# Optimization experiments

Measured on AMD Instinct MI355X. Metric: run time of the kernel, lower is better.

## Reference

```python
import jax, jax.numpy as jnp
import numpy as np

B, L, V, E_ENC, D_DEC, E_EMB = 256, 128, 4096, 1024, 1024, 512


def _lin(key, out_f, in_f, scale=0.02):
    k1, k2 = jax.random.split(key)
    return (jax.random.normal(k1, (out_f, in_f), jnp.float32) * scale,
            jax.random.normal(k2, (out_f,), jnp.float32) * scale)


def setup_inputs() -> dict:
    key = jax.random.key(0)
    ks = jax.random.split(key, 12)
    x = jax.random.normal(ks[0], (B, 1, V), jnp.float32)
    hidden = jax.random.normal(ks[1], (1, B, D_DEC), jnp.float32)
    enc_output = jax.random.normal(ks[2], (B, L, E_ENC), jnp.float32)
    W1_w, W1_b = _lin(ks[3], D_DEC, E_ENC)
    W2_w, W2_b = _lin(ks[4], D_DEC, D_DEC)
    V_w, V_b = _lin(ks[5], 1, D_DEC)
    out2emb_w, out2emb_b = _lin(ks[6], E_EMB, V)
    gru_wi, gru_bi = _lin(ks[7], 3 * D_DEC, E_EMB + E_ENC)
    gru_wh, gru_bh = _lin(ks[8], 3 * D_DEC, D_DEC)
    fc1_w, fc1_b = _lin(ks[9], E_EMB, D_DEC)
    fc2_w, fc2_b = _lin(ks[10], V, E_EMB)
    return dict(x=x, hidden=hidden, enc_output=enc_output,
                W1_w=W1_w, W1_b=W1_b, W2_w=W2_w, W2_b=W2_b, V_w=V_w, V_b=V_b,
                out2emb_w=out2emb_w, out2emb_b=out2emb_b,
                gru_wi=gru_wi, gru_wh=gru_wh, gru_bi=gru_bi, gru_bh=gru_bh,
                fc1_w=fc1_w, fc1_b=fc1_b, fc2_w=fc2_w, fc2_b=fc2_b)


def reference(x, hidden, enc_output, W1_w, W1_b, W2_w, W2_b, V_w, V_b,
              out2emb_w, out2emb_b, gru_wi, gru_wh, gru_bi, gru_bh,
              fc1_w, fc1_b, fc2_w, fc2_b):
    # --- Bahdanau additive attention ---
    h_t = hidden[-1][:, None, :]                                   # (B,1,dec)
    score = jnp.tanh(enc_output @ W1_w.T + W1_b + h_t @ W2_w.T + W2_b)  # (B,L,dec)
    attn = jax.nn.softmax(score @ V_w.T + V_b, axis=1)             # (B,L,1)
    context = jnp.sum(attn * enc_output, axis=1)                   # (B,enc)
    # --- embed previous output distribution ---
    x_emb = x @ out2emb_w.T + out2emb_b                            # (B,1,emb)
    rnn_in = jnp.concatenate([context[:, None, :], x_emb], -1)[:, 0, :]  # (B,emb+enc)
    # --- single GRU step (PyTorch gate layout r,z,n) ---
    h0 = hidden[0]
    gi = rnn_in @ gru_wi.T + gru_bi
    gh = h0 @ gru_wh.T + gru_bh
    ir, iz, inn = jnp.split(gi, 3, axis=-1)
    hr, hz, hn = jnp.split(gh, 3, axis=-1)
    r = jax.nn.sigmoid(ir + hr)
    z = jax.nn.sigmoid(iz + hz)
    n = jnp.tanh(inn + r * hn)
    h_new = (1.0 - z) * n + z * h0                                 # (B,dec)
    # --- output MLP ---
    out = jnp.tanh(h_new @ fc1_w.T + fc1_b) @ fc2_w.T + fc2_b      # (B,vocab)
    return out, h_new[None], attn
```

## Files before the change

### kernel.cpp

```cpp
#include <hip/hip_runtime.h>
#include <math.h>


#define B_   256
#define L_   128
#define V_   4096
#define ENC_ 1024
#define DEC_ 1024
#define EMB_ 512
#define MB_  1048576ull

typedef __bf16 bf16;
typedef __bf16 bf16x8 __attribute__((ext_vector_type(8)));
typedef __bf16 bf16x4 __attribute__((ext_vector_type(4)));
typedef float  f32x4  __attribute__((ext_vector_type(4)));

__device__ __forceinline__ float fast_tanh(float x) {
  float e = __builtin_amdgcn_exp2f(x * 2.88539008177792681472f);
  return 1.0f - 2.0f * __builtin_amdgcn_rcpf(e + 1.0f);
}
__device__ __forceinline__ float fast_sigmoid(float x) {
  return __builtin_amdgcn_rcpf(1.0f + __builtin_amdgcn_exp2f(-1.44269504088896f * x));
}

__device__ __forceinline__ void cp16(const void* g, void* l) {
  __builtin_amdgcn_global_load_lds(
      (const __attribute__((address_space(1))) void*)g,
      (__attribute__((address_space(3))) void*)l,
      16, 0, 0);
}

__device__ __forceinline__ bf16x8 ld8f(const float* f) {
  f32x4 a = *(const f32x4*)f;
  f32x4 b = *(const f32x4*)(f + 4);
  bf16x8 r;
  r[0] = (bf16)a[0]; r[1] = (bf16)a[1]; r[2] = (bf16)a[2]; r[3] = (bf16)a[3];
  r[4] = (bf16)b[0]; r[5] = (bf16)b[1]; r[6] = (bf16)b[2]; r[7] = (bf16)b[3];
  return r;
}


__device__ __forceinline__ void gemm64_f32(
    const float* __restrict__ A, const float* __restrict__ Brow,
    int strideA, int strideB, int kbeg, int kend, int row0,
    bf16* As, bf16* Bs, f32x4 acc[4])
{
  const int t   = threadIdx.x;
  const int lane = t & 63, w = t >> 6, q = lane >> 4, c16 = lane & 15;
  const int sr  = t >> 3, lb = t & 7;

  for (int k0 = kbeg; k0 < kend; k0 += 64) {
    bf16x8 va[2], vb[2];
#pragma unroll
    for (int ch = 0; ch < 2; ch++) {
      int r    = ch * 32 + sr;
      int gcol = k0 + ((lb ^ (r & 7)) << 3);
      va[ch] = ld8f(A    + (size_t)(row0 + r) * strideA + gcol);
      vb[ch] = ld8f(Brow + (size_t)r * strideB + gcol);
    }
#pragma unroll
    for (int ch = 0; ch < 2; ch++) {
      *(bf16x8*)&As[ch * 2048 + t * 8] = va[ch];
      *(bf16x8*)&Bs[ch * 2048 + t * 8] = vb[ch];
    }
    __syncthreads();
#pragma unroll
    for (int kkb = 0; kkb < 8; kkb += 4) {
      int rb = w * 16 + c16;
      bf16x8 bfr = *(const bf16x8*)&Bs[rb * 64 + (((kkb + q) ^ (rb & 7)) << 3)];
#pragma unroll
      for (int i = 0; i < 4; i++) {
        int ra = i * 16 + c16;
        bf16x8 af = *(const bf16x8*)&As[ra * 64 + (((kkb + q) ^ (ra & 7)) << 3)];
        acc[i] = __builtin_amdgcn_mfma_f32_16x16x32_bf16(af, bfr, acc[i], 0, 0, 0);
      }
    }
    __syncthreads();
  }
}

__global__ __launch_bounds__(256) void setup_k(
    const float* __restrict__ hidden, const float* __restrict__ W2,
    const float* __restrict__ wh, const float* __restrict__ W1_b,
    const float* __restrict__ W2_b, const float* __restrict__ gbh,
    const float* __restrict__ x, const float* __restrict__ o2e,
    const float* __restrict__ enc, const float* __restrict__ W1,
    const float* __restrict__ wi, const float* __restrict__ fc1w,
    const float* __restrict__ fc2w,
    bf16* __restrict__ enc_bf, bf16* __restrict__ W1_bf,
    bf16* __restrict__ wi_bf, bf16* __restrict__ fc1_bf,
    bf16* __restrict__ fc2_bf,
    bf16* __restrict__ u, bf16* __restrict__ gh, float* __restrict__ xe4)
{
  __shared__ __align__(16) bf16 As[64 * 64];
  __shared__ __align__(16) bf16 Bs[64 * 64];

  const int bid = blockIdx.x;
  const int t   = threadIdx.x;

  if (bid >= 384) {
    int i = bid - 384;
    const float* src; bf16* dst; int blk;
    if      (i < 8192) { src = enc;  dst = enc_bf; blk = i; }
    else if (i < 8448) { src = W1;   dst = W1_bf;  blk = i - 8192; }
    else if (i < 9600) { src = wi;   dst = wi_bf;  blk = i - 8448; }
    else if (i < 9728) { src = fc1w; dst = fc1_bf; blk = i - 9600; }
    else               { src = fc2w; dst = fc2_bf; blk = i - 9728; }
    const size_t base = (size_t)blk * 4096 + t * 16;
    const float* s = src + base;
    bf16* d = dst + base;
    *(bf16x8*)(d)     = ld8f(s);
    *(bf16x8*)(d + 8) = ld8f(s + 8);
    return;
  }

  const int lane = t & 63, w = t >> 6, q = lane >> 4, c16 = lane & 15;
  f32x4 acc[4] = {};

  if (bid < 256) {
    const int row0 = (bid >> 6) * 64;
    const int col0 = (bid & 63) * 64;
    const bool isU = (col0 < 1024);
    const float* Brow = isU ? (W2 + (size_t)col0 * 1024)
                            : (wh + (size_t)(col0 - 1024) * 1024);
    gemm64_f32(hidden, Brow, 1024, 1024, 0, 1024, row0, As, Bs, acc);

    const int gc = col0 + w * 16 + c16;
    float bias = isU ? (W1_b[gc] + W2_b[gc]) : gbh[gc - 1024];
#pragma unroll
    for (int i = 0; i < 4; i++) {
      int gr0 = row0 + i * 16 + q * 4;
#pragma unroll
      for (int r = 0; r < 4; r++) {
        float v = acc[i][r] + bias;
        if (isU) u[(size_t)(gr0 + r) * 1024 + gc] = (bf16)v;
        else     gh[(size_t)(gr0 + r) * 3072 + (gc - 1024)] = (bf16)v;
      }
    }
  } else {
    const int i3   = bid - 256;
    const int col0 = (i3 & 7) * 64;
    const int row0 = ((i3 >> 3) & 3) * 64;
    const int z    = i3 >> 5;
    gemm64_f32(x, o2e + (size_t)col0 * 4096, 4096, 4096,
               z * 1024, z * 1024 + 1024, row0, As, Bs, acc);

    const int gc = col0 + w * 16 + c16;
    float* out = xe4 + (size_t)z * 131072;
#pragma unroll
    for (int i = 0; i < 4; i++) {
      int gr0 = row0 + i * 16 + q * 4;
#pragma unroll
      for (int r = 0; r < 4; r++)
        out[(size_t)(gr0 + r) * 512 + gc] = acc[i][r];
    }
  }
}

__device__ __forceinline__ void stage_tile256(
    const bf16* __restrict__ A, const bf16* __restrict__ Bw,
    bf16* As, bf16* Bs, int row0, int col0, int k0, int t)
{
  const int sr = t >> 3, lb = t & 7;
#pragma unroll
  for (int ch = 0; ch < 4; ch++) {
    int r    = ch * 64 + sr;
    int gcol = k0 + ((lb ^ (r & 7)) << 3);
    cp16(A  + (size_t)(row0 + r) * 1024 + gcol, &As[r * 64 + lb * 8]);
    cp16(Bw + (size_t)(col0 + r) * 1024 + gcol, &Bs[r * 64 + lb * 8]);
  }
}

__global__ __launch_bounds__(512, 2) void score_8p(
    const bf16* __restrict__ A,
    const bf16* __restrict__ Bw,
    const bf16* __restrict__ u,
    const float* __restrict__ Vw,
    float* __restrict__ e_part)
{
  __shared__ __align__(16) bf16 sA[2 * 16384];
  __shared__ __align__(16) bf16 sB[2 * 16384];
  __shared__ float s_part[4][256];

  const int t = threadIdx.x;
  const int wg  = blockIdx.x;
  const int swz = (wg & 7) * 64 + (wg >> 3);
  const int bx  = swz & 3;
  const int by  = swz >> 2;
  const int row0 = by * 256;
  const int col0 = bx * 256;

  const int lane = t & 63, w = t >> 6;
  const int wm = w >> 2, wn = w & 3;
  const int q = lane >> 4, c16 = lane & 15;

  stage_tile256(A, Bw, sA, sB, row0, col0, 0, t);
  stage_tile256(A, Bw, sA + 16384, sB + 16384, row0, col0, 64, t);
  asm volatile("s_waitcnt vmcnt(8)" ::: "memory");
  __builtin_amdgcn_s_barrier();

  f32x4 acc[8][4] = {};

  for (int kt = 0; kt < 16; ++kt) {
    const bf16* As = sA + (kt & 1) * 16384;
    const bf16* Bs = sB + (kt & 1) * 16384;

    bf16x8 bfr[2][4];
#pragma unroll
    for (int j = 0; j < 4; j++) {
      const int rb = wn * 64 + j * 16 + c16;
      bfr[0][j] = *(const bf16x8*)&Bs[rb * 64 + (((0 + q) ^ (rb & 7)) << 3)];
      bfr[1][j] = *(const bf16x8*)&Bs[rb * 64 + (((4 + q) ^ (rb & 7)) << 3)];
    }
    __builtin_amdgcn_s_setprio(1);
#pragma unroll
    for (int i = 0; i < 8; i++) {
      const int ra = wm * 128 + i * 16 + c16;
      bf16x8 a0 = *(const bf16x8*)&As[ra * 64 + (((0 + q) ^ (ra & 7)) << 3)];
      bf16x8 a1 = *(const bf16x8*)&As[ra * 64 + (((4 + q) ^ (ra & 7)) << 3)];
#pragma unroll
      for (int j = 0; j < 4; j++)
        acc[i][j] = __builtin_amdgcn_mfma_f32_16x16x32_bf16(a0, bfr[0][j], acc[i][j], 0, 0, 0);
#pragma unroll
      for (int j = 0; j < 4; j++)
        acc[i][j] = __builtin_amdgcn_mfma_f32_16x16x32_bf16(a1, bfr[1][j], acc[i][j], 0, 0, 0);
    }
    __builtin_amdgcn_s_setprio(0);
    __builtin_amdgcn_s_barrier();
    if (kt < 14) {
      stage_tile256(A, Bw, sA + (kt & 1) * 16384, sB + (kt & 1) * 16384,
                    row0, col0, (kt + 2) * 64, t);
      asm volatile("s_waitcnt vmcnt(8)" ::: "memory");
    } else {
      asm volatile("s_waitcnt vmcnt(0)" ::: "memory");
    }
    __builtin_amdgcn_s_barrier();
  }

  const int b = by * 2 + wm;
  float uc[4], vw[4];
#pragma unroll
  for (int j = 0; j < 4; j++) {
    const int gc = col0 + wn * 64 + j * 16 + c16;
    uc[j] = (float)u[b * 1024 + gc];
    vw[j] = Vw[gc];
  }
#pragma unroll
  for (int i = 0; i < 8; i++) {
#pragma unroll
    for (int r = 0; r < 4; r++) {
      float v = 0.0f;
#pragma unroll
      for (int j = 0; j < 4; j++)
        v += fast_tanh(acc[i][j][r] + uc[j]) * vw[j];
      v += __shfl_xor(v, 1);
      v += __shfl_xor(v, 2);
      v += __shfl_xor(v, 4);
      v += __shfl_xor(v, 8);
      if (c16 == 0) s_part[wn][wm * 128 + i * 16 + q * 4 + r] = v;
    }
  }
  __syncthreads();
  if (t < 256)
    e_part[(size_t)bx * 32768 + row0 + t] =
        s_part[0][t] + s_part[1][t] + s_part[2][t] + s_part[3][t];
}

__global__ __launch_bounds__(256) void softmax_f(
    const float* __restrict__ e_part,
    const bf16* __restrict__ enc,
    const float* __restrict__ xe4,
    const float* __restrict__ o2eb,
    float* __restrict__ attn_out,
    bf16* __restrict__ rnn_in)
{
  const int b = blockIdx.x;
  const int t = threadIdx.x;
  __shared__ float se[128];

  if (t < 128) {
    float s = 0.0f;
#pragma unroll
    for (int cb = 0; cb < 4; cb++) s += e_part[(size_t)cb * 32768 + b * 128 + t];
    se[t] = s;
  }
  __syncthreads();

  float m = -1e30f;
  for (int l = 0; l < 128; l++) m = fmaxf(m, se[l]);
  float sum = 0.0f;
  for (int l = 0; l < 128; l++) sum += expf(se[l] - m);
  float inv = 1.0f / sum;
  __syncthreads();
  if (t < 128) {
    float p = expf(se[t] - m) * inv;
    attn_out[b * 128 + t] = p;
    se[t] = p;
  }
  __syncthreads();

  float a0 = 0, a1 = 0, a2 = 0, a3 = 0;
  const bf16* ep = enc + (size_t)b * L_ * ENC_ + t * 4;
  for (int l = 0; l < 128; l++) {
    float p = se[l];
    bf16x4 v = *(const bf16x4*)(ep + (size_t)l * ENC_);
    a0 += p * (float)v[0]; a1 += p * (float)v[1];
    a2 += p * (float)v[2]; a3 += p * (float)v[3];
  }
  bf16x4 o;
  o[0] = (bf16)a0; o[1] = (bf16)a1; o[2] = (bf16)a2; o[3] = (bf16)a3;
  *(bf16x4*)(rnn_in + (size_t)b * 1536 + t * 4) = o;

#pragma unroll
  for (int jj = 0; jj < 2; jj++) {
    int j = jj * 256 + t;
    float v = o2eb[j];
#pragma unroll
    for (int z = 0; z < 4; z++) v += xe4[(size_t)z * 131072 + b * 512 + j];
    rnn_in[(size_t)b * 1536 + 1024 + j] = (bf16)v;
  }
}

template <int ACT, int OUTF32>
__global__ __launch_bounds__(256) void gemm_f(
    const bf16* __restrict__ A, const bf16* __restrict__ Bw,
    const float* __restrict__ bias1,
    void* __restrict__ C, int K, int out_ld)
{
  __shared__ __align__(16) bf16 As[64 * 64];
  __shared__ __align__(16) bf16 Bs[64 * 64];

  const int t    = threadIdx.x;
  const int lane = t & 63;
  const int w    = t >> 6;
  const int q    = lane >> 4;
  const int c16  = lane & 15;
  const int sr   = t >> 3;
  const int lb   = t & 7;
  const int row0 = blockIdx.y * 64;
  const int col0 = blockIdx.x * 64;

  f32x4 acc[4] = {};

  for (int k0 = 0; k0 < K; k0 += 64) {
#pragma unroll
    for (int ch = 0; ch < 2; ch++) {
      int r    = ch * 32 + sr;
      int gcol = k0 + ((lb ^ (r & 7)) << 3);
      cp16(A  + (size_t)(row0 + r) * K + gcol, &As[ch * 2048 + t * 8]);
      cp16(Bw + (size_t)(col0 + r) * K + gcol, &Bs[ch * 2048 + t * 8]);
    }
    __syncthreads();
#pragma unroll
    for (int kkb = 0; kkb < 8; kkb += 4) {
      int rb = w * 16 + c16;
      bf16x8 bfr = *(const bf16x8*)&Bs[rb * 64 + (((kkb + q) ^ (rb & 7)) << 3)];
#pragma unroll
      for (int i = 0; i < 4; i++) {
        int ra = i * 16 + c16;
        bf16x8 af = *(const bf16x8*)&As[ra * 64 + (((kkb + q) ^ (ra & 7)) << 3)];
        acc[i] = __builtin_amdgcn_mfma_f32_16x16x32_bf16(af, bfr, acc[i], 0, 0, 0);
      }
    }
    __syncthreads();
  }

  const int gc = col0 + w * 16 + c16;
  float bias = bias1[gc];
#pragma unroll
  for (int i = 0; i < 4; i++) {
    int gr0 = row0 + i * 16 + q * 4;
#pragma unroll
    for (int r = 0; r < 4; r++) {
      float v = acc[i][r] + bias;
      if (ACT == 1) v = fast_tanh(v);
      size_t off = (size_t)(gr0 + r) * out_ld + gc;
      if (OUTF32) ((float*)C)[off] = v;
      else        ((bf16*)C)[off] = (bf16)v;
    }
  }
}

__global__ __launch_bounds__(256) void gru_f(
    const bf16* __restrict__ gi, const bf16* __restrict__ gh,
    const float* __restrict__ h0,
    float* __restrict__ hnew_out, bf16* __restrict__ hnew_i)
{
  int idx = blockIdx.x * 256 + threadIdx.x;
  int b = idx >> 10, d = idx & 1023;
  const bf16* gib = gi + b * 3072;
  const bf16* ghb = gh + b * 3072;
  float ir = (float)gib[d], iz = (float)gib[1024 + d], in = (float)gib[2048 + d];
  float hr = (float)ghb[d], hz = (float)ghb[1024 + d], hn = (float)ghb[2048 + d];
  float r = fast_sigmoid(ir + hr);
  float z = fast_sigmoid(iz + hz);
  float n = fast_tanh(in + r * hn);
  float h = (1.0f - z) * n + z * h0[idx];
  hnew_out[idx] = h;
  hnew_i[idx]   = (bf16)h;
}

extern "C" void kernel_launch(void* const* d_in, const int* in_sizes, int n_in,
                              void* d_out, int out_size, void* d_ws, size_t ws_size,
                              hipStream_t stream) {
  const float* x      = (const float*)d_in[0];
  const float* hidden = (const float*)d_in[1];
  const float* enc    = (const float*)d_in[2];
  const float* W1_w   = (const float*)d_in[3];
  const float* W1_b   = (const float*)d_in[4];
  const float* W2_w   = (const float*)d_in[5];
  const float* W2_b   = (const float*)d_in[6];
  const float* V_w    = (const float*)d_in[7];
  const float* o2e_w  = (const float*)d_in[9];
  const float* o2e_b  = (const float*)d_in[10];
  const float* gru_wi = (const float*)d_in[11];
  const float* gru_wh = (const float*)d_in[12];
  const float* gru_bi = (const float*)d_in[13];
  const float* gru_bh = (const float*)d_in[14];
  const float* fc1_w  = (const float*)d_in[15];
  const float* fc1_b  = (const float*)d_in[16];
  const float* fc2_w  = (const float*)d_in[17];
  const float* fc2_b  = (const float*)d_in[18];

  float* out_main = (float*)d_out;
  float* out_h    = out_main + (size_t)B_ * V_;
  float* out_attn = out_h + (size_t)B_ * DEC_;

  char* ws = (char*)d_ws;
  bf16*  enc_bf  = (bf16*)(ws);
  bf16*  W1_bf   = (bf16*)(ws + 64 * MB_);
  bf16*  wi_bf   = (bf16*)(ws + 66 * MB_);
  bf16*  fc1_bf  = (bf16*)(ws + 75 * MB_);
  bf16*  fc2_bf  = (bf16*)(ws + 76 * MB_);
  bf16*  u_bf    = (bf16*)(ws + 80 * MB_);
  bf16*  gh_bf   = (bf16*)(ws + 80 * MB_ + 524288);
  float* e_part  = (float*)(ws + 82 * MB_);
  bf16*  gi_bf   = (bf16*)(ws + 82 * MB_ + 524288);
  bf16*  rnn_in  = (bf16*)(ws + 84 * MB_);
  bf16*  tbuf    = (bf16*)(ws + 84 * MB_ + 786432);
  bf16*  hnew_bf = (bf16*)(ws + 85 * MB_);
  float* xe4     = (float*)(ws + 85 * MB_ + 524288);

  setup_k<<<10624, 256, 0, stream>>>(
      hidden, W2_w, gru_wh, W1_b, W2_b, gru_bh, x, o2e_w,
      enc, W1_w, gru_wi, fc1_w, fc2_w,
      enc_bf, W1_bf, wi_bf, fc1_bf, fc2_bf, u_bf, gh_bf, xe4);

  score_8p<<<512, 512, 0, stream>>>(enc_bf, W1_bf, u_bf, V_w, e_part);

  softmax_f<<<B_, 256, 0, stream>>>(e_part, enc_bf, xe4, o2e_b, out_attn, rnn_in);

  gemm_f<0, 0><<<dim3(48, 4), 256, 0, stream>>>(rnn_in, wi_bf, gru_bi, gi_bf, 1536, 3072);

  gru_f<<<(B_ * DEC_) / 256, 256, 0, stream>>>(gi_bf, gh_bf, hidden, out_h, hnew_bf);

  gemm_f<1, 0><<<dim3(8, 4), 256, 0, stream>>>(hnew_bf, fc1_bf, fc1_b, tbuf, 1024, 512);

  gemm_f<0, 1><<<dim3(64, 4), 256, 0, stream>>>(tbuf, fc2_bf, fc2_b, out_main, 512, 4096);
}
```

Baseline: 416.4 us.

## Interleave half-tile global loads with MFMA phases in score GEMM main loop

Restructures the 256x256 score GEMM K-loop into four sub-phases. Each phase loads a fragment slice from LDS, issues one half-tile global-to-LDS copy, then runs a 4x4 block of MFMAs under raised priority. The A operand is now prefetched one tile ahead and B two tiles ahead, with barriers and scheduling fences between phases. The aim is to hide global load latency and LDS traffic behind matrix work. The cost is more barriers per iteration and trickier buffer-reuse correctness.

```diff
diff --git a/kernel.cpp b/kernel.cpp
--- a/kernel.cpp
+++ b/kernel.cpp
@@ -157,19 +157,22 @@
   }
 }
 
-__device__ __forceinline__ void stage_tile256(
-    const bf16* __restrict__ A, const bf16* __restrict__ Bw,
-    bf16* As, bf16* Bs, int row0, int col0, int k0, int t)
+__device__ __forceinline__ void stage_half(
+    const bf16* __restrict__ src, bf16* dst, int grow0, int k0, int t)
 {
   const int sr = t >> 3, lb = t & 7;
 #pragma unroll
-  for (int ch = 0; ch < 4; ch++) {
+  for (int ch = 0; ch < 2; ch++) {
     int r    = ch * 64 + sr;
     int gcol = k0 + ((lb ^ (r & 7)) << 3);
-    cp16(A  + (size_t)(row0 + r) * 1024 + gcol, &As[r * 64 + lb * 8]);
-    cp16(Bw + (size_t)(col0 + r) * 1024 + gcol, &Bs[r * 64 + lb * 8]);
-  }
-}
+    cp16(src + (size_t)(grow0 + r) * 1024 + gcol, dst + r * 64 + lb * 8);
+  }
+}
+
+#define BAR()   __builtin_amdgcn_s_barrier()
+#define LGKM0() { asm volatile("s_waitcnt lgkmcnt(0)" ::: "memory"); \
+                  __builtin_amdgcn_sched_barrier(0); }
+#define SB0()   __builtin_amdgcn_sched_barrier(0)
 
 __global__ __launch_bounds__(512, 2) void score_8p(
     const bf16* __restrict__ A,
@@ -194,47 +197,106 @@
   const int wm = w >> 2, wn = w & 3;
   const int q = lane >> 4, c16 = lane & 15;
 
-  stage_tile256(A, Bw, sA, sB, row0, col0, 0, t);
-  stage_tile256(A, Bw, sA + 16384, sB + 16384, row0, col0, 64, t);
-  asm volatile("s_waitcnt vmcnt(8)" ::: "memory");
-  __builtin_amdgcn_s_barrier();
+  stage_half(A,  sA,          row0,       0,  t);
+  stage_half(A,  sA + 8192,   row0 + 128, 0,  t);
+  stage_half(Bw, sB,          col0,       0,  t);
+  stage_half(Bw, sB + 8192,   col0 + 128, 0,  t);
+  stage_half(Bw, sB + 16384,        col0,       64, t);
+  stage_half(Bw, sB + 16384 + 8192, col0 + 128, 64, t);
+  asm volatile("s_waitcnt vmcnt(4)" ::: "memory");
+  BAR(); SB0();
 
   f32x4 acc[8][4] = {};
 
+  const int rb_base = wn * 64 + c16;
+  const int ra_base = wm * 128 + c16;
+
   for (int kt = 0; kt < 16; ++kt) {
-    const bf16* As = sA + (kt & 1) * 16384;
-    const bf16* Bs = sB + (kt & 1) * 16384;
-
-    bf16x8 bfr[2][4];
+    const int cur = kt & 1;
+    const bf16* As = sA + cur * 16384;
+    const bf16* Bs = sB + cur * 16384;
+    bf16* Anx = sA + (1 - cur) * 16384;
+    bf16* Bnx = sB + cur * 16384;
+    const bool stA = (kt < 15);
+    const bool stB = (kt < 14);
+
+    bf16x8 bfr0[4], bfr1[4], af[4];
+
 #pragma unroll
     for (int j = 0; j < 4; j++) {
-      const int rb = wn * 64 + j * 16 + c16;
-      bfr[0][j] = *(const bf16x8*)&Bs[rb * 64 + (((0 + q) ^ (rb & 7)) << 3)];
-      bfr[1][j] = *(const bf16x8*)&Bs[rb * 64 + (((4 + q) ^ (rb & 7)) << 3)];
-    }
+      const int rb = rb_base + j * 16;
+      bfr0[j] = *(const bf16x8*)&Bs[rb * 64 + ((q ^ (rb & 7)) << 3)];
+    }
+#pragma unroll
+    for (int i = 0; i < 4; i++) {
+      const int ra = ra_base + i * 16;
+      af[i] = *(const bf16x8*)&As[ra * 64 + ((q ^ (ra & 7)) << 3)];
+    }
+    if (stA) stage_half(A, Anx, row0, (kt + 1) * 64, t);
+    BAR(); LGKM0();
     __builtin_amdgcn_s_setprio(1);
 #pragma unroll
-    for (int i = 0; i < 8; i++) {
-      const int ra = wm * 128 + i * 16 + c16;
-      bf16x8 a0 = *(const bf16x8*)&As[ra * 64 + (((0 + q) ^ (ra & 7)) << 3)];
-      bf16x8 a1 = *(const bf16x8*)&As[ra * 64 + (((4 + q) ^ (ra & 7)) << 3)];
+    for (int i = 0; i < 4; i++)
 #pragma unroll
       for (int j = 0; j < 4; j++)
-        acc[i][j] = __builtin_amdgcn_mfma_f32_16x16x32_bf16(a0, bfr[0][j], acc[i][j], 0, 0, 0);
+        acc[i][j] = __builtin_amdgcn_mfma_f32_16x16x32_bf16(af[i], bfr0[j], acc[i][j], 0, 0, 0);
+    __builtin_amdgcn_s_setprio(0);
+    BAR(); SB0();
+
+#pragma unroll
+    for (int j = 0; j < 4; j++) {
+      const int rb = rb_base + j * 16;
+      bfr1[j] = *(const bf16x8*)&Bs[rb * 64 + (((4 + q) ^ (rb & 7)) << 3)];
+    }
+#pragma unroll
+    for (int i = 0; i < 4; i++) {
+      const int ra = ra_base + i * 16;
+      af[i] = *(const bf16x8*)&As[ra * 64 + (((4 + q) ^ (ra & 7)) << 3)];
+    }
+    if (stA) stage_half(A, Anx + 8192, row0 + 128, (kt + 1) * 64, t);
+    BAR(); LGKM0();
+    __builtin_amdgcn_s_setprio(1);
+#pragma unroll
+    for (int i = 0; i < 4; i++)
 #pragma unroll
       for (int j = 0; j < 4; j++)
-        acc[i][j] = __builtin_amdgcn_mfma_f32_16x16x32_bf16(a1, bfr[1][j], acc[i][j], 0, 0, 0);
-    }
+        acc[i][j] = __builtin_amdgcn_mfma_f32_16x16x32_bf16(af[i], bfr1[j], acc[i][j], 0, 0, 0);
     __builtin_amdgcn_s_setprio(0);
-    __builtin_amdgcn_s_barrier();
-    if (kt < 14) {
-      stage_tile256(A, Bw, sA + (kt & 1) * 16384, sB + (kt & 1) * 16384,
-                    row0, col0, (kt + 2) * 64, t);
-      asm volatile("s_waitcnt vmcnt(8)" ::: "memory");
-    } else {
-      asm volatile("s_waitcnt vmcnt(0)" ::: "memory");
-    }
-    __builtin_amdgcn_s_barrier();
+    BAR(); SB0();
+
+#pragma unroll
+    for (int i = 0; i < 4; i++) {
+      const int ra = ra_base + (i + 4) * 16;
+      af[i] = *(const bf16x8*)&As[ra * 64 + ((q ^ (ra & 7)) << 3)];
+    }
+    if (stB) stage_half(Bw, Bnx, col0, (kt + 2) * 64, t);
+    BAR(); LGKM0();
+    __builtin_amdgcn_s_setprio(1);
+#pragma unroll
+    for (int i = 0; i < 4; i++)
+#pragma unroll
+      for (int j = 0; j < 4; j++)
+        acc[i + 4][j] = __builtin_amdgcn_mfma_f32_16x16x32_bf16(af[i], bfr0[j], acc[i + 4][j], 0, 0, 0);
+    __builtin_amdgcn_s_setprio(0);
+    BAR(); SB0();
+
+#pragma unroll
+    for (int i = 0; i < 4; i++) {
+      const int ra = ra_base + (i + 4) * 16;
+      af[i] = *(const bf16x8*)&As[ra * 64 + (((4 + q) ^ (ra & 7)) << 3)];
+    }
+    if (stB) stage_half(Bw, Bnx + 8192, col0 + 128, (kt + 2) * 64, t);
+    BAR(); LGKM0();
+    __builtin_amdgcn_s_setprio(1);
+#pragma unroll
+    for (int i = 0; i < 4; i++)
+#pragma unroll
+      for (int j = 0; j < 4; j++)
+        acc[i + 4][j] = __builtin_amdgcn_mfma_f32_16x16x32_bf16(af[i], bfr1[j], acc[i + 4][j], 0, 0, 0);
+    __builtin_amdgcn_s_setprio(0);
+    if (kt < 14) { asm volatile("s_waitcnt vmcnt(4)" ::: "memory"); }
+    else         { asm volatile("s_waitcnt vmcnt(0)" ::: "memory"); }
+    BAR(); SB0();
   }
 
   const int b = by * 2 + wm;
```

Result: faster. 407.5 us (-2.2%).

## Restructure score GEMM main loop into fine-grained interleaved LDS/global pipeline

Applied to the files above, without the earlier changes.

Rewrites the score_8p K-loop as an 8-phase software pipeline over half-tiles. Global-to-LDS copies of A and B halves are issued between MFMA groups, and LDS fragment reads are double-buffered in registers using explicit lgkmcnt/vmcnt waits and sched_barriers. The goal is to hide LDS read latency and global load latency behind MFMA work instead of stalling at per-k-tile barriers. The trade-off is many more barriers, fragile hand-tuned wait counts and higher register pressure. The epilogue also buffers the reduced row sums in registers before the LDS stores.

```diff
diff --git a/kernel.cpp b/kernel.cpp
--- a/kernel.cpp
+++ b/kernel.cpp
@@ -157,19 +157,43 @@
   }
 }
 
-__device__ __forceinline__ void stage_tile256(
-    const bf16* __restrict__ A, const bf16* __restrict__ Bw,
-    bf16* As, bf16* Bs, int row0, int col0, int k0, int t)
+__device__ __forceinline__ void stage_half(
+    const bf16* __restrict__ src, bf16* dst, int grow0, int k0, int t)
 {
   const int sr = t >> 3, lb = t & 7;
 #pragma unroll
-  for (int ch = 0; ch < 4; ch++) {
+  for (int ch = 0; ch < 2; ch++) {
     int r    = ch * 64 + sr;
     int gcol = k0 + ((lb ^ (r & 7)) << 3);
-    cp16(A  + (size_t)(row0 + r) * 1024 + gcol, &As[r * 64 + lb * 8]);
-    cp16(Bw + (size_t)(col0 + r) * 1024 + gcol, &Bs[r * 64 + lb * 8]);
-  }
-}
+    cp16(src + (size_t)(grow0 + r) * 1024 + gcol, dst + r * 64 + lb * 8);
+  }
+}
+
+#define BAR()   __builtin_amdgcn_s_barrier()
+#define SB0()   __builtin_amdgcn_sched_barrier(0)
+#define LGKM8() { asm volatile("s_waitcnt lgkmcnt(8)" ::: "memory"); SB0(); }
+#define LGKM4() { asm volatile("s_waitcnt lgkmcnt(4)" ::: "memory"); SB0(); }
+#define LGKM0() { asm volatile("s_waitcnt lgkmcnt(0)" ::: "memory"); SB0(); }
+#define VM2()   asm volatile("s_waitcnt vmcnt(2)" ::: "memory")
+#define VM4()   asm volatile("s_waitcnt vmcnt(4)" ::: "memory")
+
+#define RD_A4(dst, base, ib, kq)                                            \
+  _Pragma("unroll") for (int i = 0; i < 4; i++) {                           \
+    const int ra = ra_base + ((ib) + i) * 16;                               \
+    dst[i] = *(const bf16x8*)&(base)[ra * 64 + (((kq) ^ (ra & 7)) << 3)];   \
+  }
+#define RD_B4(dst, base, kq)                                                \
+  _Pragma("unroll") for (int j = 0; j < 4; j++) {                           \
+    const int rb = rb_base + j * 16;                                        \
+    dst[j] = *(const bf16x8*)&(base)[rb * 64 + (((kq) ^ (rb & 7)) << 3)];   \
+  }
+#define MFMA16(ib, afv, bv)                                                 \
+  __builtin_amdgcn_s_setprio(1);                                            \
+  _Pragma("unroll") for (int i = 0; i < 4; i++)                             \
+    _Pragma("unroll") for (int j = 0; j < 4; j++)                           \
+      acc[(ib) + i][j] = __builtin_amdgcn_mfma_f32_16x16x32_bf16(           \
+          afv[i], bv[j], acc[(ib) + i][j], 0, 0, 0);                        \
+  __builtin_amdgcn_s_setprio(0);
 
 __global__ __launch_bounds__(512, 2) void score_8p(
     const bf16* __restrict__ A,
@@ -178,8 +202,10 @@
     const float* __restrict__ Vw,
     float* __restrict__ e_part)
 {
-  __shared__ __align__(16) bf16 sA[2 * 16384];
-  __shared__ __align__(16) bf16 sB[2 * 16384];
+  __shared__ __align__(16) bf16 sA0[16384];
+  __shared__ __align__(16) bf16 sA1[16384];
+  __shared__ __align__(16) bf16 sB0[16384];
+  __shared__ __align__(16) bf16 sB1[16384];
   __shared__ float s_part[4][256];
 
   const int t = threadIdx.x;
@@ -193,48 +219,84 @@
   const int lane = t & 63, w = t >> 6;
   const int wm = w >> 2, wn = w & 3;
   const int q = lane >> 4, c16 = lane & 15;
-
-  stage_tile256(A, Bw, sA, sB, row0, col0, 0, t);
-  stage_tile256(A, Bw, sA + 16384, sB + 16384, row0, col0, 64, t);
-  asm volatile("s_waitcnt vmcnt(8)" ::: "memory");
-  __builtin_amdgcn_s_barrier();
-
+  const int rb_base = wn * 64 + c16;
+  const int ra_base = wm * 128 + c16;
+
+  bf16x8 afA[4], afB[4], b0[4], b1[4];
   f32x4 acc[8][4] = {};
 
-  for (int kt = 0; kt < 16; ++kt) {
-    const bf16* As = sA + (kt & 1) * 16384;
-    const bf16* Bs = sB + (kt & 1) * 16384;
-
-    bf16x8 bfr[2][4];
-#pragma unroll
-    for (int j = 0; j < 4; j++) {
-      const int rb = wn * 64 + j * 16 + c16;
-      bfr[0][j] = *(const bf16x8*)&Bs[rb * 64 + (((0 + q) ^ (rb & 7)) << 3)];
-      bfr[1][j] = *(const bf16x8*)&Bs[rb * 64 + (((4 + q) ^ (rb & 7)) << 3)];
-    }
-    __builtin_amdgcn_s_setprio(1);
-#pragma unroll
-    for (int i = 0; i < 8; i++) {
-      const int ra = wm * 128 + i * 16 + c16;
-      bf16x8 a0 = *(const bf16x8*)&As[ra * 64 + (((0 + q) ^ (ra & 7)) << 3)];
-      bf16x8 a1 = *(const bf16x8*)&As[ra * 64 + (((4 + q) ^ (ra & 7)) << 3)];
-#pragma unroll
-      for (int j = 0; j < 4; j++)
-        acc[i][j] = __builtin_amdgcn_mfma_f32_16x16x32_bf16(a0, bfr[0][j], acc[i][j], 0, 0, 0);
-#pragma unroll
-      for (int j = 0; j < 4; j++)
-        acc[i][j] = __builtin_amdgcn_mfma_f32_16x16x32_bf16(a1, bfr[1][j], acc[i][j], 0, 0, 0);
-    }
-    __builtin_amdgcn_s_setprio(0);
-    __builtin_amdgcn_s_barrier();
-    if (kt < 14) {
-      stage_tile256(A, Bw, sA + (kt & 1) * 16384, sB + (kt & 1) * 16384,
-                    row0, col0, (kt + 2) * 64, t);
-      asm volatile("s_waitcnt vmcnt(8)" ::: "memory");
+  stage_half(A,  sA0,        row0,       0,  t);
+  stage_half(A,  sA0 + 8192, row0 + 128, 0,  t);
+  stage_half(Bw, sB0,        col0,       0,  t);
+  stage_half(Bw, sB0 + 8192, col0 + 128, 0,  t);
+  stage_half(Bw, sB1,        col0,       64, t);
+  stage_half(Bw, sB1 + 8192, col0 + 128, 64, t);
+  VM4();
+  BAR(); SB0();
+  RD_A4(afA, sA0, 0, q);
+  RD_B4(b0, sB0, q);
+
+  for (int k = 0; k < 8; ++k) {
+    const int e = 2 * k, o = 2 * k + 1;
+    const bool nl = (k < 7);
+
+    RD_A4(afB, sA0, 0, 4 + q);
+    RD_B4(b1, sB0, 4 + q);
+    stage_half(A, sA1, row0, o * 64, t);
+    LGKM8();
+    MFMA16(0, afA, b0);
+    BAR();
+
+    RD_A4(afA, sA0, 4, q);
+    stage_half(A, sA1 + 8192, row0 + 128, o * 64, t);
+    LGKM4();
+    MFMA16(0, afB, b1);
+    BAR();
+
+    RD_A4(afB, sA0, 4, 4 + q);
+    if (nl) stage_half(Bw, sB0, col0, (e + 2) * 64, t);
+    LGKM4();
+    MFMA16(4, afA, b0);
+    VM2();
+    BAR();
+
+    RD_A4(afA, sA1, 0, q);
+    RD_B4(b0, sB1, q);
+    if (nl) stage_half(Bw, sB0 + 8192, col0 + 128, (e + 2) * 64, t);
+    LGKM8();
+    MFMA16(4, afB, b1);
+    BAR();
+
+    RD_A4(afB, sA1, 0, 4 + q);
+    RD_B4(b1, sB1, 4 + q);
+    if (nl) stage_half(A, sA0, row0, (e + 2) * 64, t);
+    LGKM8();
+    MFMA16(0, afA, b0);
+    BAR();
+
+    RD_A4(afA, sA1, 4, q);
+    if (nl) stage_half(A, sA0 + 8192, row0 + 128, (e + 2) * 64, t);
+    LGKM4();
+    MFMA16(0, afB, b1);
+    BAR();
+
+    RD_A4(afB, sA1, 4, 4 + q);
+    if (nl) stage_half(Bw, sB1, col0, (o + 2) * 64, t);
+    LGKM4();
+    MFMA16(4, afA, b0);
+    VM2();
+    BAR();
+
+    if (nl) {
+      RD_A4(afA, sA0, 0, q);
+      RD_B4(b0, sB0, q);
+      stage_half(Bw, sB1 + 8192, col0 + 128, (o + 2) * 64, t);
+      LGKM8();
     } else {
-      asm volatile("s_waitcnt vmcnt(0)" ::: "memory");
-    }
-    __builtin_amdgcn_s_barrier();
+      LGKM0();
+    }
+    MFMA16(4, afB, b1);
+    BAR();
   }
 
   const int b = by * 2 + wm;
@@ -245,6 +307,7 @@
     uc[j] = (float)u[b * 1024 + gc];
     vw[j] = Vw[gc];
   }
+  float rsum[8][4];
 #pragma unroll
   for (int i = 0; i < 8; i++) {
 #pragma unroll
@@ -257,9 +320,14 @@
       v += __shfl_xor(v, 2);
       v += __shfl_xor(v, 4);
       v += __shfl_xor(v, 8);
-      if (c16 == 0) s_part[wn][wm * 128 + i * 16 + q * 4 + r] = v;
-    }
-  }
+      rsum[i][r] = v;
+    }
+  }
+#pragma unroll
+  for (int i = 0; i < 8; i++)
+#pragma unroll
+    for (int r = 0; r < 4; r++)
+      if (c16 == 0) s_part[wn][wm * 128 + i * 16 + q * 4 + r] = rsum[i][r];
   __syncthreads();
   if (t < 256)
     e_part[(size_t)bx * 32768 + row0 + t] =
```

Result: no change. 412.6 us (-0.9%).
